# Performance work log

Measured on AMD Instinct MI355X. Metric: run time of the kernel, lower is better.

Reference implementation:

```python
import jax, jax.numpy as jnp
import numpy as np

ALPHA = 0.1  # config['alpha']


def setup_inputs() -> dict:
    key = jax.random.key(0)
    k1, k2, k3, k4, k5 = jax.random.split(key, 5)
    n_bs, bit, n_cls, class_bit, n_train = 128, 48, 100, 16, 10000
    u = jax.random.normal(k1, (n_bs, bit), dtype=jnp.float32)
    # multi-hot labels (float, as in torch: y.float())
    y = jax.random.bernoulli(k2, 0.1, (n_bs, n_cls)).astype(jnp.float32)
    ind = jnp.arange(n_bs, dtype=jnp.int64)  # distinct in-range row indices
    # buffers mid-training: U holds previous class-wise codes, Y previous labels
    U = jax.random.normal(k3, (n_train, n_cls, class_bit), dtype=jnp.float32) * 0.1
    Y = jax.random.bernoulli(k4, 0.1, (n_train, n_cls)).astype(jnp.float32)
    # xavier_uniform-like init for w_D [n_class, bit, class_bit]
    limit = np.sqrt(6.0 / (bit + class_bit)).astype(np.float32)
    w_D = jax.random.uniform(k5, (n_cls, bit, class_bit), dtype=jnp.float32,
                             minval=-limit, maxval=limit)
    return {"u": u, "y": y, "ind": ind, "U": U, "Y": Y, "w_D": w_D}


def reference(u, y, ind, U, Y, w_D):
    # update label buffer: self.Y[ind, :] = y
    Y = Y.at[ind].set(y)
    # u_ = matmul(u, w_D).permute(1,0,2): [n_bs, n_cls, class_bit]
    u_ = jnp.einsum('bk,ckd->bcd', u, w_D)
    # update code buffer with detached u_ (torch: self.U[ind] = u_.data)
    U = U.at[ind].set(jax.lax.stop_gradient(u_))
    # pairwise similarity s: [n_bs, n_train, n_cls]
    s = y[:, None, :] * Y[None, :, :]
    # inner_product: sum over class_bit -> [n_bs, n_train, n_cls]
    ip = jnp.einsum('tcd,bcd->btc', U, u_)
    # stable log(1 + exp(ip)) - s*ip, exactly as the torch expression
    likelihood = (jnp.log1p(jnp.exp(-jnp.abs(ip))) + jnp.maximum(ip, 0.0)
                  - s * ip).mean()
    quantization = ALPHA * jnp.mean((u_ - jnp.sign(u_)) ** 2)
    return likelihood + quantization
```

## Files before the change

kernel.cpp:

```cpp
#include <hip/hip_runtime.h>
#include <math.h>

#define CB 16
#define ALPHA 0.1f
#define LOG2E 1.4426950408889634f
#define LN2F  0.6931471805599453f
#define MAXW 8
#define N_BS 128
#define BIT  48

typedef __bf16 bf16x8 __attribute__((ext_vector_type(8)));
typedef float  f32x16 __attribute__((ext_vector_type(16)));

__device__ __forceinline__ unsigned int f2bf(float x) {
    unsigned int v = __float_as_uint(x);
    return (v + 0x7FFFu + ((v >> 16) & 1u)) >> 16;
}

__global__ __launch_bounds__(256, 4) void loss_fused(
        const float* __restrict__ u, const float* __restrict__ y,
        const float* __restrict__ w_D,
        const float* __restrict__ U, const float* __restrict__ Yb,
        const int* __restrict__ ind,
        float* __restrict__ partials, float* __restrict__ quant_partials,
        int n_cls, int n_train, int ntile, int GY) {
    __shared__ unsigned int ubf32[4 * N_BS * 9];
    __shared__ int pflag[MAXW * 32];

    const int tid  = threadIdx.x;
    const int lane = tid & 63;
    const int wid  = tid >> 6;
    const int bx   = blockIdx.x;
    const int by   = blockIdx.y;
    const int c    = bx * 4 + wid;
    const int r    = lane & 31;
    const int h    = lane >> 5;
    const int nw   = (ntile - by + GY - 1) / GY;

    pflag[tid] = -1;
    __syncthreads();
    if (tid < N_BS) {
        int t = ind[tid];
        for (int w = 0; w < nw; ++w) {
            unsigned rl = (unsigned)(t - (by + w * GY) * 32);
            if (rl < 32u) pflag[w * 32 + rl] = tid;
        }
    }

    float acc0[8] = {0,0,0,0,0,0,0,0};
    float acc1[8] = {0,0,0,0,0,0,0,0};
    float acc2[8] = {0,0,0,0,0,0,0,0};
    float acc3[8] = {0,0,0,0,0,0,0,0};
    {
        const float* __restrict__ wdc = w_D + (size_t)c * BIT * CB + h * 8;
        const float* __restrict__ ub0p = u + (size_t)(0 * 32 + r) * BIT;
        const float* __restrict__ ub1p = u + (size_t)(1 * 32 + r) * BIT;
        const float* __restrict__ ub2p = u + (size_t)(2 * 32 + r) * BIT;
        const float* __restrict__ ub3p = u + (size_t)(3 * 32 + r) * BIT;
        for (int k4 = 0; k4 < BIT / 4; ++k4) {
            float4 ub0 = *(const float4*)(ub0p + k4 * 4);
            float4 ub1 = *(const float4*)(ub1p + k4 * 4);
            float4 ub2 = *(const float4*)(ub2p + k4 * 4);
            float4 ub3 = *(const float4*)(ub3p + k4 * 4);
            #pragma unroll
            for (int kk = 0; kk < 4; ++kk) {
                const float* wrow = wdc + (k4 * 4 + kk) * CB;
                float4 wa = *(const float4*)(wrow);
                float4 wb = *(const float4*)(wrow + 4);
                float w8[8];
                w8[0]=wa.x; w8[1]=wa.y; w8[2]=wa.z; w8[3]=wa.w;
                w8[4]=wb.x; w8[5]=wb.y; w8[6]=wb.z; w8[7]=wb.w;
                float s0 = (&ub0.x)[kk], s1 = (&ub1.x)[kk];
                float s2 = (&ub2.x)[kk], s3 = (&ub3.x)[kk];
                #pragma unroll
                for (int j = 0; j < 8; ++j) {
                    acc0[j] = fmaf(s0, w8[j], acc0[j]);
                    acc1[j] = fmaf(s1, w8[j], acc1[j]);
                    acc2[j] = fmaf(s2, w8[j], acc2[j]);
                    acc3[j] = fmaf(s3, w8[j], acc3[j]);
                }
            }
        }
    }

    if (by == 0) {
        float q = 0.f;
        #pragma unroll
        for (int j = 0; j < 8; ++j) {
            float v, sgn, d;
            v = acc0[j]; sgn = (v>0.f)?1.f:((v<0.f)?-1.f:0.f); d = v-sgn; q = fmaf(d,d,q);
            v = acc1[j]; sgn = (v>0.f)?1.f:((v<0.f)?-1.f:0.f); d = v-sgn; q = fmaf(d,d,q);
            v = acc2[j]; sgn = (v>0.f)?1.f:((v<0.f)?-1.f:0.f); d = v-sgn; q = fmaf(d,d,q);
            v = acc3[j]; sgn = (v>0.f)?1.f:((v<0.f)?-1.f:0.f); d = v-sgn; q = fmaf(d,d,q);
        }
        #pragma unroll
        for (int off = 32; off > 0; off >>= 1) q += __shfl_down(q, off, 64);
        if (lane == 0) quant_partials[bx * 4 + wid] = q;
    }

    float ypc0 = y[(size_t)(0 * 32 + r) * n_cls + c];
    float ypc1 = y[(size_t)(1 * 32 + r) * n_cls + c];
    float ypc2 = y[(size_t)(2 * 32 + r) * n_cls + c];
    float ypc3 = y[(size_t)(3 * 32 + r) * n_cls + c];
    float vv[8], ww[8];
    #pragma unroll
    for (int j = 0; j < 8; ++j) {
        ww[j] = acc0[j] + acc1[j] + acc2[j] + acc3[j];
        vv[j] = ypc0*acc0[j] + ypc1*acc1[j] + ypc2*acc2[j] + ypc3*acc3[j];
    }
    #pragma unroll
    for (int m = 1; m < 32; m <<= 1) {
        #pragma unroll
        for (int j = 0; j < 8; ++j) {
            vv[j] += __shfl_xor(vv[j], m, 64);
            ww[j] += __shfl_xor(ww[j], m, 64);
        }
    }

    {
        unsigned int* d0 = &ubf32[(wid * N_BS + 0 * 32 + r) * 9 + h * 4];
        unsigned int* d1 = &ubf32[(wid * N_BS + 1 * 32 + r) * 9 + h * 4];
        unsigned int* d2 = &ubf32[(wid * N_BS + 2 * 32 + r) * 9 + h * 4];
        unsigned int* d3 = &ubf32[(wid * N_BS + 3 * 32 + r) * 9 + h * 4];
        #pragma unroll
        for (int j2 = 0; j2 < 4; ++j2) {
            d0[j2] = f2bf(acc0[2*j2]) | (f2bf(acc0[2*j2+1]) << 16);
            d1[j2] = f2bf(acc1[2*j2]) | (f2bf(acc1[2*j2+1]) << 16);
            d2[j2] = f2bf(acc2[2*j2]) | (f2bf(acc2[2*j2+1]) << 16);
            d3[j2] = f2bf(acc3[2*j2]) | (f2bf(acc3[2*j2+1]) << 16);
        }
    }

    bf16x8 B0, B1, B2, B3;
    #pragma unroll
    for (int j = 0; j < 8; ++j) {
        B0[j] = (__bf16)(acc0[j] * LOG2E);
        B1[j] = (__bf16)(acc1[j] * LOG2E);
        B2[j] = (__bf16)(acc2[j] * LOG2E);
        B3[j] = (__bf16)(acc3[j] * LOG2E);
    }

    __syncthreads();

    float acc = 0.f;
    f32x16 zc = {};
    #pragma unroll 1
    for (int w = 0; w < nw; ++w) {
        const int t0  = (by + w * GY) * 32;
        const int row = t0 + r;
        const int rc  = (row < n_train) ? row : (n_train - 1);
        const float* __restrict__ ar = U + ((size_t)rc * n_cls + c) * CB + h * 8;
        float4 a0 = *(const float4*)(ar);
        float4 a1 = *(const float4*)(ar + 4);
        float Yv = Yb[(size_t)rc * n_cls + c];

        const int pf = pflag[w * 32 + r];
        if (pf >= 0) {
            const unsigned int* src = &ubf32[(wid * N_BS + pf) * 9 + h * 4];
            unsigned int w0 = src[0], w1 = src[1], w2 = src[2], w3 = src[3];
            a0.x = __uint_as_float(w0 << 16);
            a0.y = __uint_as_float(w0 & 0xFFFF0000u);
            a0.z = __uint_as_float(w1 << 16);
            a0.w = __uint_as_float(w1 & 0xFFFF0000u);
            a1.x = __uint_as_float(w2 << 16);
            a1.y = __uint_as_float(w2 & 0xFFFF0000u);
            a1.z = __uint_as_float(w3 << 16);
            a1.w = __uint_as_float(w3 & 0xFFFF0000u);
            Yv = y[(size_t)pf * n_cls + c];
        }
        if (row >= n_train) {
            a0 = make_float4(0.f, 0.f, 0.f, 0.f); a1 = a0; Yv = 0.f;
        }

        float sv = a0.x*vv[0] + a0.y*vv[1] + a0.z*vv[2] + a0.w*vv[3]
                 + a1.x*vv[4] + a1.y*vv[5] + a1.z*vv[6] + a1.w*vv[7];
        float sw = a0.x*ww[0] + a0.y*ww[1] + a0.z*ww[2] + a0.w*ww[3]
                 + a1.x*ww[4] + a1.y*ww[5] + a1.z*ww[6] + a1.w*ww[7];

        bf16x8 A;
        A[0] = (__bf16)a0.x; A[1] = (__bf16)a0.y;
        A[2] = (__bf16)a0.z; A[3] = (__bf16)a0.w;
        A[4] = (__bf16)a1.x; A[5] = (__bf16)a1.y;
        A[6] = (__bf16)a1.z; A[7] = (__bf16)a1.w;

        float accA = 0.f;
        float pp   = 1.f;
        #pragma unroll
        for (int bt = 0; bt < 4; ++bt) {
            bf16x8 Bf = (bt == 0) ? B0 : (bt == 1) ? B1 : (bt == 2) ? B2 : B3;
            f32x16 D = __builtin_amdgcn_mfma_f32_32x32x16_bf16(A, Bf, zc,
                                                               0, 0, 0);
            float a[16];
            #pragma unroll
            for (int j = 0; j < 16; ++j) {
                float ipa = fabsf(D[j]);
                a[j] = 1.0f + __builtin_amdgcn_exp2f(-ipa);
                accA += ipa;
            }
            #pragma unroll
            for (int s = 1; s < 16; s <<= 1)
                #pragma unroll
                for (int j = 0; j < 16; j += 2 * s) a[j] *= a[j + s];
            pp *= a[0];
        }
        float accL = __builtin_amdgcn_logf(pp);
        acc += LN2F * accL + (0.5f * LN2F) * accA + 0.5f * sw - Yv * sv;
    }

    #pragma unroll
    for (int off = 32; off > 0; off >>= 1)
        acc += __shfl_down(acc, off, 64);
    if (lane == 0) {
        int bid = by * gridDim.x + bx;
        partials[bid * 4 + wid] = acc;
    }
}

__global__ __launch_bounds__(256) void finalize_kernel(
        const float* __restrict__ partials, int nblk,
        const float* __restrict__ quant_partials, int n_quant,
        float* __restrict__ out, double pad_corr,
        double like_scale, double quant_scale) {
    double s = 0.0, q = 0.0;
    for (int i = threadIdx.x; i < nblk; i += 256) s += (double)partials[i];
    for (int i = threadIdx.x; i < n_quant; i += 256) q += (double)quant_partials[i];
    #pragma unroll
    for (int off = 32; off > 0; off >>= 1) {
        s += __shfl_down(s, off, 64);
        q += __shfl_down(q, off, 64);
    }
    __shared__ double dred[4][2];
    int lane = threadIdx.x & 63, wid = threadIdx.x >> 6;
    if (lane == 0) { dred[wid][0] = s; dred[wid][1] = q; }
    __syncthreads();
    if (threadIdx.x == 0) {
        double S = dred[0][0] + dred[1][0] + dred[2][0] + dred[3][0];
        double Q = dred[0][1] + dred[1][1] + dred[2][1] + dred[3][1];
        out[0] = (float)((S - pad_corr) * like_scale + Q * quant_scale);
    }
}

extern "C" void kernel_launch(void* const* d_in, const int* in_sizes, int n_in,
                              void* d_out, int out_size, void* d_ws, size_t ws_size,
                              hipStream_t stream) {
    const float* u   = (const float*)d_in[0];
    const float* y   = (const float*)d_in[1];
    const int*   ind = (const int*)d_in[2];
    const float* U   = (const float*)d_in[3];
    const float* Yb  = (const float*)d_in[4];
    const float* w_D = (const float*)d_in[5];

    const int n_bs    = in_sizes[2];
    const int n_cls   = in_sizes[1] / n_bs;
    const int n_train = in_sizes[4] / n_cls;

    const int totalU = n_bs * n_cls * CB;
    const int ntile  = (n_train + 31) / 32;
    const int GY     = (ntile + MAXW - 1) / MAXW;
    const int gx     = (n_cls + 3) / 4;
    const int nblk   = GY * gx;
    const int npart  = nblk * 4;
    const int nquant = gx * 4;

    char* ws = (char*)d_ws;
    size_t off = 0;
    float* partials = (float*)(ws + off);        off += (size_t)npart * 4;
    float* quant_partials = (float*)(ws + off);  off += (size_t)nquant * 4;

    loss_fused<<<dim3(gx, GY), 256, 0, stream>>>(
        u, y, w_D, U, Yb, ind, partials, quant_partials,
        n_cls, n_train, ntile, GY);

    const double ln2 = 0.6931471805599453;
    const double n_pad = (double)((long long)(ntile * 32 - n_train) *
                                  (long long)n_bs * (long long)n_cls);
    const double pad_corr    = ln2 * n_pad;
    const double like_scale  = 1.0 / ((double)n_bs * n_train * n_cls);
    const double quant_scale = (double)ALPHA / (double)totalU;

    finalize_kernel<<<1, 256, 0, stream>>>(partials, npart,
                                           quant_partials, nquant,
                                           (float*)d_out, pad_corr,
                                           like_scale, quant_scale);
}
```

Before: 58.49 us.

## Stage u and w_D as bf16 in LDS and use packed FMA for projection

The kernel now cooperatively loads u and the block's w_D slice into shared memory as packed bf16 before the projection, instead of having every wave read them from global memory as fp32. The projection uses two-wide packed float math, and the shared buffer is reused for the bf16 code stash behind an extra barrier. The product tree for the log term becomes a serial running product, and MAXW shrinks to 4. This cuts redundant global traffic and instruction count in the prologue, but rounding u and w_D to bf16 reduces the accuracy of u_, and the serial product adds a longer dependency chain.

```diff
diff --git a/kernel.cpp b/kernel.cpp
--- a/kernel.cpp
+++ b/kernel.cpp
@@ -5,16 +5,23 @@
 #define ALPHA 0.1f
 #define LOG2E 1.4426950408889634f
 #define LN2F  0.6931471805599453f
-#define MAXW 8
+#define MAXW 4
 #define N_BS 128
 #define BIT  48
 
 typedef __bf16 bf16x8 __attribute__((ext_vector_type(8)));
 typedef float  f32x16 __attribute__((ext_vector_type(16)));
+typedef float  f32x2  __attribute__((ext_vector_type(2)));
 
 __device__ __forceinline__ unsigned int f2bf(float x) {
     unsigned int v = __float_as_uint(x);
     return (v + 0x7FFFu + ((v >> 16) & 1u)) >> 16;
+}
+__device__ __forceinline__ f32x2 bfup2(unsigned int p) {
+    f32x2 r;
+    r.x = __uint_as_float(p << 16);
+    r.y = __uint_as_float(p & 0xFFFF0000u);
+    return r;
 }
 
 __global__ __launch_bounds__(256, 4) void loss_fused(
@@ -24,8 +31,11 @@
         const int* __restrict__ ind,
         float* __restrict__ partials, float* __restrict__ quant_partials,
         int n_cls, int n_train, int ntile, int GY) {
-    __shared__ unsigned int ubf32[4 * N_BS * 9];
+    __shared__ unsigned int smem[4736];
     __shared__ int pflag[MAXW * 32];
+    unsigned int* u_st  = smem;
+    unsigned int* wd_st = smem + 3200;
+    unsigned int* ubf32 = smem;
 
     const int tid  = threadIdx.x;
     const int lane = tid & 63;
@@ -37,8 +47,24 @@
     const int h    = lane >> 5;
     const int nw   = (ntile - by + GY - 1) / GY;
 
-    pflag[tid] = -1;
+    if (tid < MAXW * 32) pflag[tid] = -1;
+    #pragma unroll
+    for (int it = 0; it < 12; ++it) {
+        int f = it * 256 + tid;
+        int b = f / 24, k2 = f % 24;
+        float2 uv = *(const float2*)(u + (size_t)b * BIT + k2 * 2);
+        u_st[b * 25 + k2] = f2bf(uv.x) | (f2bf(uv.y) << 16);
+    }
+    #pragma unroll
+    for (int it = 0; it < 6; ++it) {
+        int f = it * 256 + tid;
+        int cc = f / 384, rest = f % 384;
+        float2 wv = *(const float2*)(w_D + (size_t)(bx * 4 + cc) * BIT * CB
+                                     + rest * 2);
+        wd_st[f] = f2bf(wv.x) | (f2bf(wv.y) << 16);
+    }
     __syncthreads();
+
     if (tid < N_BS) {
         int t = ind[tid];
         for (int w = 0; w < nw; ++w) {
@@ -47,38 +73,40 @@
         }
     }
 
-    float acc0[8] = {0,0,0,0,0,0,0,0};
-    float acc1[8] = {0,0,0,0,0,0,0,0};
-    float acc2[8] = {0,0,0,0,0,0,0,0};
-    float acc3[8] = {0,0,0,0,0,0,0,0};
+    f32x2 acc0[4] = {}; f32x2 acc1[4] = {};
+    f32x2 acc2[4] = {}; f32x2 acc3[4] = {};
     {
-        const float* __restrict__ wdc = w_D + (size_t)c * BIT * CB + h * 8;
-        const float* __restrict__ ub0p = u + (size_t)(0 * 32 + r) * BIT;
-        const float* __restrict__ ub1p = u + (size_t)(1 * 32 + r) * BIT;
-        const float* __restrict__ ub2p = u + (size_t)(2 * 32 + r) * BIT;
-        const float* __restrict__ ub3p = u + (size_t)(3 * 32 + r) * BIT;
-        for (int k4 = 0; k4 < BIT / 4; ++k4) {
-            float4 ub0 = *(const float4*)(ub0p + k4 * 4);
-            float4 ub1 = *(const float4*)(ub1p + k4 * 4);
-            float4 ub2 = *(const float4*)(ub2p + k4 * 4);
-            float4 ub3 = *(const float4*)(ub3p + k4 * 4);
+        const unsigned int* __restrict__ up0 = u_st + (0 * 32 + r) * 25;
+        const unsigned int* __restrict__ up1 = u_st + (1 * 32 + r) * 25;
+        const unsigned int* __restrict__ up2 = u_st + (2 * 32 + r) * 25;
+        const unsigned int* __restrict__ up3 = u_st + (3 * 32 + r) * 25;
+        const unsigned int* __restrict__ wdc = wd_st + wid * 384 + h * 4;
+        for (int k2 = 0; k2 < 24; ++k2) {
+            unsigned int p0 = up0[k2], p1 = up1[k2];
+            unsigned int p2 = up2[k2], p3 = up3[k2];
             #pragma unroll
-            for (int kk = 0; kk < 4; ++kk) {
-                const float* wrow = wdc + (k4 * 4 + kk) * CB;
-                float4 wa = *(const float4*)(wrow);
-                float4 wb = *(const float4*)(wrow + 4);
-                float w8[8];
-                w8[0]=wa.x; w8[1]=wa.y; w8[2]=wa.z; w8[3]=wa.w;
-                w8[4]=wb.x; w8[5]=wb.y; w8[6]=wb.z; w8[7]=wb.w;
-                float s0 = (&ub0.x)[kk], s1 = (&ub1.x)[kk];
-                float s2 = (&ub2.x)[kk], s3 = (&ub3.x)[kk];
-                #pragma unroll
-                for (int j = 0; j < 8; ++j) {
-                    acc0[j] = fmaf(s0, w8[j], acc0[j]);
-                    acc1[j] = fmaf(s1, w8[j], acc1[j]);
-                    acc2[j] = fmaf(s2, w8[j], acc2[j]);
-                    acc3[j] = fmaf(s3, w8[j], acc3[j]);
-                }
+            for (int kk = 0; kk < 2; ++kk) {
+                uint4 wq = *(const uint4*)(wdc + (2 * k2 + kk) * 8);
+                f32x2 w0 = bfup2(wq.x), w1 = bfup2(wq.y);
+                f32x2 w2 = bfup2(wq.z), w3 = bfup2(wq.w);
+                float s0f = kk ? __uint_as_float(p0 & 0xFFFF0000u)
+                               : __uint_as_float(p0 << 16);
+                float s1f = kk ? __uint_as_float(p1 & 0xFFFF0000u)
+                               : __uint_as_float(p1 << 16);
+                float s2f = kk ? __uint_as_float(p2 & 0xFFFF0000u)
+                               : __uint_as_float(p2 << 16);
+                float s3f = kk ? __uint_as_float(p3 & 0xFFFF0000u)
+                               : __uint_as_float(p3 << 16);
+                f32x2 s0 = {s0f, s0f}, s1 = {s1f, s1f};
+                f32x2 s2 = {s2f, s2f}, s3 = {s3f, s3f};
+                acc0[0] += s0 * w0; acc0[1] += s0 * w1;
+                acc0[2] += s0 * w2; acc0[3] += s0 * w3;
+                acc1[0] += s1 * w0; acc1[1] += s1 * w1;
+                acc1[2] += s1 * w2; acc1[3] += s1 * w3;
+                acc2[0] += s2 * w0; acc2[1] += s2 * w1;
+                acc2[2] += s2 * w2; acc2[3] += s2 * w3;
+                acc3[0] += s3 * w0; acc3[1] += s3 * w1;
+                acc3[2] += s3 * w2; acc3[3] += s3 * w3;
             }
         }
     }
@@ -86,12 +114,16 @@
     if (by == 0) {
         float q = 0.f;
         #pragma unroll
-        for (int j = 0; j < 8; ++j) {
-            float v, sgn, d;
-            v = acc0[j]; sgn = (v>0.f)?1.f:((v<0.f)?-1.f:0.f); d = v-sgn; q = fmaf(d,d,q);
-            v = acc1[j]; sgn = (v>0.f)?1.f:((v<0.f)?-1.f:0.f); d = v-sgn; q = fmaf(d,d,q);
-            v = acc2[j]; sgn = (v>0.f)?1.f:((v<0.f)?-1.f:0.f); d = v-sgn; q = fmaf(d,d,q);
-            v = acc3[j]; sgn = (v>0.f)?1.f:((v<0.f)?-1.f:0.f); d = v-sgn; q = fmaf(d,d,q);
+        for (int j2 = 0; j2 < 4; ++j2) {
+            float vb[8] = {acc0[j2].x, acc0[j2].y, acc1[j2].x, acc1[j2].y,
+                           acc2[j2].x, acc2[j2].y, acc3[j2].x, acc3[j2].y};
+            #pragma unroll
+            for (int i = 0; i < 8; ++i) {
+                float v = vb[i];
+                float sg = (v > 0.f) ? 1.f : ((v < 0.f) ? -1.f : 0.f);
+                float d = v - sg;
+                q = fmaf(d, d, q);
+            }
         }
         #pragma unroll
         for (int off = 32; off > 0; off >>= 1) q += __shfl_down(q, off, 64);
@@ -102,20 +134,45 @@
     float ypc1 = y[(size_t)(1 * 32 + r) * n_cls + c];
     float ypc2 = y[(size_t)(2 * 32 + r) * n_cls + c];
     float ypc3 = y[(size_t)(3 * 32 + r) * n_cls + c];
-    float vv[8], ww[8];
-    #pragma unroll
-    for (int j = 0; j < 8; ++j) {
-        ww[j] = acc0[j] + acc1[j] + acc2[j] + acc3[j];
-        vv[j] = ypc0*acc0[j] + ypc1*acc1[j] + ypc2*acc2[j] + ypc3*acc3[j];
+    f32x2 y0 = {ypc0, ypc0}, y1 = {ypc1, ypc1};
+    f32x2 y2 = {ypc2, ypc2}, y3 = {ypc3, ypc3};
+    f32x2 vv[4], ww[4];
+    #pragma unroll
+    for (int j2 = 0; j2 < 4; ++j2) {
+        ww[j2] = acc0[j2] + acc1[j2] + acc2[j2] + acc3[j2];
+        vv[j2] = y0 * acc0[j2] + y1 * acc1[j2] + y2 * acc2[j2] + y3 * acc3[j2];
     }
     #pragma unroll
     for (int m = 1; m < 32; m <<= 1) {
         #pragma unroll
-        for (int j = 0; j < 8; ++j) {
-            vv[j] += __shfl_xor(vv[j], m, 64);
-            ww[j] += __shfl_xor(ww[j], m, 64);
-        }
-    }
+        for (int j2 = 0; j2 < 4; ++j2) {
+            vv[j2].x += __shfl_xor(vv[j2].x, m, 64);
+            vv[j2].y += __shfl_xor(vv[j2].y, m, 64);
+            ww[j2].x += __shfl_xor(ww[j2].x, m, 64);
+            ww[j2].y += __shfl_xor(ww[j2].y, m, 64);
+        }
+    }
+    float vvf[8], wwf[8];
+    #pragma unroll
+    for (int j2 = 0; j2 < 4; ++j2) {
+        vvf[2 * j2] = vv[j2].x; vvf[2 * j2 + 1] = vv[j2].y;
+        wwf[2 * j2] = ww[j2].x; wwf[2 * j2 + 1] = ww[j2].y;
+    }
+
+    bf16x8 B0, B1, B2, B3;
+    #pragma unroll
+    for (int j2 = 0; j2 < 4; ++j2) {
+        B0[2 * j2] = (__bf16)(acc0[j2].x * LOG2E);
+        B0[2 * j2 + 1] = (__bf16)(acc0[j2].y * LOG2E);
+        B1[2 * j2] = (__bf16)(acc1[j2].x * LOG2E);
+        B1[2 * j2 + 1] = (__bf16)(acc1[j2].y * LOG2E);
+        B2[2 * j2] = (__bf16)(acc2[j2].x * LOG2E);
+        B2[2 * j2 + 1] = (__bf16)(acc2[j2].y * LOG2E);
+        B3[2 * j2] = (__bf16)(acc3[j2].x * LOG2E);
+        B3[2 * j2 + 1] = (__bf16)(acc3[j2].y * LOG2E);
+    }
+
+    __syncthreads();
 
     {
         unsigned int* d0 = &ubf32[(wid * N_BS + 0 * 32 + r) * 9 + h * 4];
@@ -124,22 +181,12 @@
         unsigned int* d3 = &ubf32[(wid * N_BS + 3 * 32 + r) * 9 + h * 4];
         #pragma unroll
         for (int j2 = 0; j2 < 4; ++j2) {
-            d0[j2] = f2bf(acc0[2*j2]) | (f2bf(acc0[2*j2+1]) << 16);
-            d1[j2] = f2bf(acc1[2*j2]) | (f2bf(acc1[2*j2+1]) << 16);
-            d2[j2] = f2bf(acc2[2*j2]) | (f2bf(acc2[2*j2+1]) << 16);
-            d3[j2] = f2bf(acc3[2*j2]) | (f2bf(acc3[2*j2+1]) << 16);
-        }
-    }
-
-    bf16x8 B0, B1, B2, B3;
-    #pragma unroll
-    for (int j = 0; j < 8; ++j) {
-        B0[j] = (__bf16)(acc0[j] * LOG2E);
-        B1[j] = (__bf16)(acc1[j] * LOG2E);
-        B2[j] = (__bf16)(acc2[j] * LOG2E);
-        B3[j] = (__bf16)(acc3[j] * LOG2E);
-    }
-
+            d0[j2] = f2bf(acc0[j2].x) | (f2bf(acc0[j2].y) << 16);
+            d1[j2] = f2bf(acc1[j2].x) | (f2bf(acc1[j2].y) << 16);
+            d2[j2] = f2bf(acc2[j2].x) | (f2bf(acc2[j2].y) << 16);
+            d3[j2] = f2bf(acc3[j2].x) | (f2bf(acc3[j2].y) << 16);
+        }
+    }
     __syncthreads();
 
     float acc = 0.f;
@@ -172,10 +219,10 @@
             a0 = make_float4(0.f, 0.f, 0.f, 0.f); a1 = a0; Yv = 0.f;
         }
 
-        float sv = a0.x*vv[0] + a0.y*vv[1] + a0.z*vv[2] + a0.w*vv[3]
-                 + a1.x*vv[4] + a1.y*vv[5] + a1.z*vv[6] + a1.w*vv[7];
-        float sw = a0.x*ww[0] + a0.y*ww[1] + a0.z*ww[2] + a0.w*ww[3]
-                 + a1.x*ww[4] + a1.y*ww[5] + a1.z*ww[6] + a1.w*ww[7];
+        float sv = a0.x*vvf[0] + a0.y*vvf[1] + a0.z*vvf[2] + a0.w*vvf[3]
+                 + a1.x*vvf[4] + a1.y*vvf[5] + a1.z*vvf[6] + a1.w*vvf[7];
+        float sw = a0.x*wwf[0] + a0.y*wwf[1] + a0.z*wwf[2] + a0.w*wwf[3]
+                 + a1.x*wwf[4] + a1.y*wwf[5] + a1.z*wwf[6] + a1.w*wwf[7];
 
         bf16x8 A;
         A[0] = (__bf16)a0.x; A[1] = (__bf16)a0.y;
@@ -190,18 +237,12 @@
             bf16x8 Bf = (bt == 0) ? B0 : (bt == 1) ? B1 : (bt == 2) ? B2 : B3;
             f32x16 D = __builtin_amdgcn_mfma_f32_32x32x16_bf16(A, Bf, zc,
                                                                0, 0, 0);
-            float a[16];
             #pragma unroll
             for (int j = 0; j < 16; ++j) {
                 float ipa = fabsf(D[j]);
-                a[j] = 1.0f + __builtin_amdgcn_exp2f(-ipa);
                 accA += ipa;
+                pp *= (1.0f + __builtin_amdgcn_exp2f(-ipa));
             }
-            #pragma unroll
-            for (int s = 1; s < 16; s <<= 1)
-                #pragma unroll
-                for (int j = 0; j < 16; j += 2 * s) a[j] *= a[j + s];
-            pp *= a[0];
         }
         float accL = __builtin_amdgcn_logf(pp);
         acc += LN2F * accL + (0.5f * LN2F) * accA + 0.5f * sw - Yv * sv;
```

New measurement: 67.51 us. 1.15x slower.

## Compute u·w_D projection with MFMA via LDS-staged bf16 weights

Applied to the files above, without the earlier changes.

Replaces the scalar FMA projection of u by w_D with bf16 MFMA instructions, staging a transposed bf16 copy of each block's w_D slice in shared memory. The per-class code slice is written to LDS from the MFMA output, and the y-weighted and plain column sums are recomputed from LDS. The LOG2E scale moves from the B operand onto the A operand, and MAXW is reduced so the pflag loop is fully unrolled. The aim is to cut the per-block prologue cost of the FP32 projection, at the price of extra LDS traffic, a wasted half of the MFMA N dimension, and bf16 rounding of u and w_D.

```diff
diff --git a/kernel.cpp b/kernel.cpp
--- a/kernel.cpp
+++ b/kernel.cpp
@@ -5,7 +5,7 @@
 #define ALPHA 0.1f
 #define LOG2E 1.4426950408889634f
 #define LN2F  0.6931471805599453f
-#define MAXW 8
+#define MAXW 4
 #define N_BS 128
 #define BIT  48
 
@@ -24,7 +24,8 @@
         const int* __restrict__ ind,
         float* __restrict__ partials, float* __restrict__ quant_partials,
         int n_cls, int n_train, int ntile, int GY) {
-    __shared__ unsigned int ubf32[4 * N_BS * 9];
+    __shared__ unsigned int slice[4 * N_BS * 9];
+    __shared__ unsigned int wdt[4 * 16 * 25];
     __shared__ int pflag[MAXW * 32];
 
     const int tid  = threadIdx.x;
@@ -37,113 +38,112 @@
     const int h    = lane >> 5;
     const int nw   = (ntile - by + GY - 1) / GY;
 
-    pflag[tid] = -1;
+    if (tid < MAXW * 32) pflag[tid] = -1;
+    unsigned short* wdt16w = (unsigned short*)wdt;
+    #pragma unroll
+    for (int it = 0; it < 12; ++it) {
+        int f = it * 256 + tid;
+        int cc = f / 768, rem = f % 768;
+        int k = rem >> 4, d = rem & 15;
+        float wv = w_D[(size_t)(bx * 4 + cc) * 768 + rem];
+        wdt16w[(cc * 16 + d) * 50 + k] = (unsigned short)f2bf(wv);
+    }
     __syncthreads();
+
     if (tid < N_BS) {
         int t = ind[tid];
-        for (int w = 0; w < nw; ++w) {
+        #pragma unroll
+        for (int w = 0; w < MAXW; ++w) {
             unsigned rl = (unsigned)(t - (by + w * GY) * 32);
             if (rl < 32u) pflag[w * 32 + rl] = tid;
         }
     }
 
-    float acc0[8] = {0,0,0,0,0,0,0,0};
-    float acc1[8] = {0,0,0,0,0,0,0,0};
-    float acc2[8] = {0,0,0,0,0,0,0,0};
-    float acc3[8] = {0,0,0,0,0,0,0,0};
+    unsigned short* sl16 = (unsigned short*)slice;
+    const int dcol = lane & 31;
+    float qacc = 0.f;
+    f32x16 zc = {};
+    #pragma unroll 1
+    for (int bt = 0; bt < 4; ++bt) {
+        const int b0 = bt * 32 + r;
+        f32x16 D = zc;
+        #pragma unroll
+        for (int kt = 0; kt < 3; ++kt) {
+            const float* __restrict__ up = u + (size_t)b0 * BIT + kt * 16 + h * 8;
+            float4 ua = *(const float4*)(up);
+            float4 ub = *(const float4*)(up + 4);
+            bf16x8 Af;
+            Af[0] = (__bf16)ua.x; Af[1] = (__bf16)ua.y;
+            Af[2] = (__bf16)ua.z; Af[3] = (__bf16)ua.w;
+            Af[4] = (__bf16)ub.x; Af[5] = (__bf16)ub.y;
+            Af[6] = (__bf16)ub.z; Af[7] = (__bf16)ub.w;
+            union { unsigned int u32[4]; bf16x8 v; } B;
+            B.u32[0] = 0; B.u32[1] = 0; B.u32[2] = 0; B.u32[3] = 0;
+            if (r < 16) {
+                const unsigned int* src = &wdt[(wid * 16 + r) * 25 + kt * 8 + h * 4];
+                B.u32[0] = src[0]; B.u32[1] = src[1];
+                B.u32[2] = src[2]; B.u32[3] = src[3];
+            }
+            D = __builtin_amdgcn_mfma_f32_32x32x16_bf16(Af, B.v, D, 0, 0, 0);
+        }
+        if (by == 0) {
+            #pragma unroll
+            for (int i = 0; i < 16; ++i) {
+                float v = D[i];
+                float sg = (v > 0.f) ? 1.f : ((v < 0.f) ? -1.f : 0.f);
+                float dd = v - sg;
+                qacc = fmaf(dd, dd, qacc);
+            }
+        }
+        if (dcol < 16) {
+            #pragma unroll
+            for (int i = 0; i < 16; ++i) {
+                int row = (i & 3) + 8 * (i >> 2) + 4 * h;
+                sl16[(wid * N_BS + bt * 32 + row) * 18 + dcol] =
+                    (unsigned short)f2bf(D[i]);
+            }
+        }
+    }
+    if (by == 0) {
+        #pragma unroll
+        for (int off = 32; off > 0; off >>= 1) qacc += __shfl_down(qacc, off, 64);
+        if (lane == 0) quant_partials[bx * 4 + wid] = qacc;
+    }
+
+    float vvf[8], wwf[8];
     {
-        const float* __restrict__ wdc = w_D + (size_t)c * BIT * CB + h * 8;
-        const float* __restrict__ ub0p = u + (size_t)(0 * 32 + r) * BIT;
-        const float* __restrict__ ub1p = u + (size_t)(1 * 32 + r) * BIT;
-        const float* __restrict__ ub2p = u + (size_t)(2 * 32 + r) * BIT;
-        const float* __restrict__ ub3p = u + (size_t)(3 * 32 + r) * BIT;
-        for (int k4 = 0; k4 < BIT / 4; ++k4) {
-            float4 ub0 = *(const float4*)(ub0p + k4 * 4);
-            float4 ub1 = *(const float4*)(ub1p + k4 * 4);
-            float4 ub2 = *(const float4*)(ub2p + k4 * 4);
-            float4 ub3 = *(const float4*)(ub3p + k4 * 4);
-            #pragma unroll
-            for (int kk = 0; kk < 4; ++kk) {
-                const float* wrow = wdc + (k4 * 4 + kk) * CB;
-                float4 wa = *(const float4*)(wrow);
-                float4 wb = *(const float4*)(wrow + 4);
-                float w8[8];
-                w8[0]=wa.x; w8[1]=wa.y; w8[2]=wa.z; w8[3]=wa.w;
-                w8[4]=wb.x; w8[5]=wb.y; w8[6]=wb.z; w8[7]=wb.w;
-                float s0 = (&ub0.x)[kk], s1 = (&ub1.x)[kk];
-                float s2 = (&ub2.x)[kk], s3 = (&ub3.x)[kk];
-                #pragma unroll
-                for (int j = 0; j < 8; ++j) {
-                    acc0[j] = fmaf(s0, w8[j], acc0[j]);
-                    acc1[j] = fmaf(s1, w8[j], acc1[j]);
-                    acc2[j] = fmaf(s2, w8[j], acc2[j]);
-                    acc3[j] = fmaf(s3, w8[j], acc3[j]);
-                }
-            }
-        }
-    }
-
-    if (by == 0) {
-        float q = 0.f;
+        const int dd = lane & 15, g = lane >> 4;
+        float vv = 0.f, ww = 0.f;
+        #pragma unroll 4
+        for (int bb = 0; bb < 32; ++bb) {
+            int b = g * 32 + bb;
+            float uv = __uint_as_float(
+                ((unsigned int)sl16[(wid * N_BS + b) * 18 + dd]) << 16);
+            ww += uv;
+            vv = fmaf(y[(size_t)b * n_cls + c], uv, vv);
+        }
+        vv += __shfl_xor(vv, 16, 64); vv += __shfl_xor(vv, 32, 64);
+        ww += __shfl_xor(ww, 16, 64); ww += __shfl_xor(ww, 32, 64);
         #pragma unroll
         for (int j = 0; j < 8; ++j) {
-            float v, sgn, d;
-            v = acc0[j]; sgn = (v>0.f)?1.f:((v<0.f)?-1.f:0.f); d = v-sgn; q = fmaf(d,d,q);
-            v = acc1[j]; sgn = (v>0.f)?1.f:((v<0.f)?-1.f:0.f); d = v-sgn; q = fmaf(d,d,q);
-            v = acc2[j]; sgn = (v>0.f)?1.f:((v<0.f)?-1.f:0.f); d = v-sgn; q = fmaf(d,d,q);
-            v = acc3[j]; sgn = (v>0.f)?1.f:((v<0.f)?-1.f:0.f); d = v-sgn; q = fmaf(d,d,q);
-        }
-        #pragma unroll
-        for (int off = 32; off > 0; off >>= 1) q += __shfl_down(q, off, 64);
-        if (lane == 0) quant_partials[bx * 4 + wid] = q;
-    }
-
-    float ypc0 = y[(size_t)(0 * 32 + r) * n_cls + c];
-    float ypc1 = y[(size_t)(1 * 32 + r) * n_cls + c];
-    float ypc2 = y[(size_t)(2 * 32 + r) * n_cls + c];
-    float ypc3 = y[(size_t)(3 * 32 + r) * n_cls + c];
-    float vv[8], ww[8];
-    #pragma unroll
-    for (int j = 0; j < 8; ++j) {
-        ww[j] = acc0[j] + acc1[j] + acc2[j] + acc3[j];
-        vv[j] = ypc0*acc0[j] + ypc1*acc1[j] + ypc2*acc2[j] + ypc3*acc3[j];
-    }
-    #pragma unroll
-    for (int m = 1; m < 32; m <<= 1) {
-        #pragma unroll
-        for (int j = 0; j < 8; ++j) {
-            vv[j] += __shfl_xor(vv[j], m, 64);
-            ww[j] += __shfl_xor(ww[j], m, 64);
-        }
-    }
-
-    {
-        unsigned int* d0 = &ubf32[(wid * N_BS + 0 * 32 + r) * 9 + h * 4];
-        unsigned int* d1 = &ubf32[(wid * N_BS + 1 * 32 + r) * 9 + h * 4];
-        unsigned int* d2 = &ubf32[(wid * N_BS + 2 * 32 + r) * 9 + h * 4];
-        unsigned int* d3 = &ubf32[(wid * N_BS + 3 * 32 + r) * 9 + h * 4];
-        #pragma unroll
-        for (int j2 = 0; j2 < 4; ++j2) {
-            d0[j2] = f2bf(acc0[2*j2]) | (f2bf(acc0[2*j2+1]) << 16);
-            d1[j2] = f2bf(acc1[2*j2]) | (f2bf(acc1[2*j2+1]) << 16);
-            d2[j2] = f2bf(acc2[2*j2]) | (f2bf(acc2[2*j2+1]) << 16);
-            d3[j2] = f2bf(acc3[2*j2]) | (f2bf(acc3[2*j2+1]) << 16);
-        }
-    }
-
-    bf16x8 B0, B1, B2, B3;
-    #pragma unroll
-    for (int j = 0; j < 8; ++j) {
-        B0[j] = (__bf16)(acc0[j] * LOG2E);
-        B1[j] = (__bf16)(acc1[j] * LOG2E);
-        B2[j] = (__bf16)(acc2[j] * LOG2E);
-        B3[j] = (__bf16)(acc3[j] * LOG2E);
+            vvf[j] = __shfl(vv, h * 8 + j, 64);
+            wwf[j] = __shfl(ww, h * 8 + j, 64);
+        }
+    }
+
+    bf16x8 BF[4];
+    #pragma unroll
+    for (int bt = 0; bt < 4; ++bt) {
+        const unsigned int* src = &slice[(wid * N_BS + bt * 32 + r) * 9 + h * 4];
+        union { unsigned int u32[4]; bf16x8 v; } B;
+        B.u32[0] = src[0]; B.u32[1] = src[1];
+        B.u32[2] = src[2]; B.u32[3] = src[3];
+        BF[bt] = B.v;
     }
 
     __syncthreads();
 
     float acc = 0.f;
-    f32x16 zc = {};
     #pragma unroll 1
     for (int w = 0; w < nw; ++w) {
         const int t0  = (by + w * GY) * 32;
@@ -156,7 +156,7 @@
 
         const int pf = pflag[w * 32 + r];
         if (pf >= 0) {
-            const unsigned int* src = &ubf32[(wid * N_BS + pf) * 9 + h * 4];
+            const unsigned int* src = &slice[(wid * N_BS + pf) * 9 + h * 4];
             unsigned int w0 = src[0], w1 = src[1], w2 = src[2], w3 = src[3];
             a0.x = __uint_as_float(w0 << 16);
             a0.y = __uint_as_float(w0 & 0xFFFF0000u);
@@ -172,36 +172,36 @@
             a0 = make_float4(0.f, 0.f, 0.f, 0.f); a1 = a0; Yv = 0.f;
         }
 
-        float sv = a0.x*vv[0] + a0.y*vv[1] + a0.z*vv[2] + a0.w*vv[3]
-                 + a1.x*vv[4] + a1.y*vv[5] + a1.z*vv[6] + a1.w*vv[7];
-        float sw = a0.x*ww[0] + a0.y*ww[1] + a0.z*ww[2] + a0.w*ww[3]
-                 + a1.x*ww[4] + a1.y*ww[5] + a1.z*ww[6] + a1.w*ww[7];
+        float sv = a0.x*vvf[0] + a0.y*vvf[1] + a0.z*vvf[2] + a0.w*vvf[3]
+                 + a1.x*vvf[4] + a1.y*vvf[5] + a1.z*vvf[6] + a1.w*vvf[7];
+        float sw = a0.x*wwf[0] + a0.y*wwf[1] + a0.z*wwf[2] + a0.w*wwf[3]
+                 + a1.x*wwf[4] + a1.y*wwf[5] + a1.z*wwf[6] + a1.w*wwf[7];
 
         bf16x8 A;
-        A[0] = (__bf16)a0.x; A[1] = (__bf16)a0.y;
-        A[2] = (__bf16)a0.z; A[3] = (__bf16)a0.w;
-        A[4] = (__bf16)a1.x; A[5] = (__bf16)a1.y;
-        A[6] = (__bf16)a1.z; A[7] = (__bf16)a1.w;
+        A[0] = (__bf16)(a0.x * LOG2E); A[1] = (__bf16)(a0.y * LOG2E);
+        A[2] = (__bf16)(a0.z * LOG2E); A[3] = (__bf16)(a0.w * LOG2E);
+        A[4] = (__bf16)(a1.x * LOG2E); A[5] = (__bf16)(a1.y * LOG2E);
+        A[6] = (__bf16)(a1.z * LOG2E); A[7] = (__bf16)(a1.w * LOG2E);
 
         float accA = 0.f;
         float pp   = 1.f;
         #pragma unroll
         for (int bt = 0; bt < 4; ++bt) {
-            bf16x8 Bf = (bt == 0) ? B0 : (bt == 1) ? B1 : (bt == 2) ? B2 : B3;
-            f32x16 D = __builtin_amdgcn_mfma_f32_32x32x16_bf16(A, Bf, zc,
+            f32x16 D = __builtin_amdgcn_mfma_f32_32x32x16_bf16(A, BF[bt], zc,
                                                                0, 0, 0);
-            float a[16];
             #pragma unroll
-            for (int j = 0; j < 16; ++j) {
-                float ipa = fabsf(D[j]);
-                a[j] = 1.0f + __builtin_amdgcn_exp2f(-ipa);
-                accA += ipa;
-            }
-            #pragma unroll
-            for (int s = 1; s < 16; s <<= 1)
+            for (int half = 0; half < 2; ++half) {
+                float a[8];
                 #pragma unroll
-                for (int j = 0; j < 16; j += 2 * s) a[j] *= a[j + s];
-            pp *= a[0];
+                for (int j = 0; j < 8; ++j) {
+                    float ipa = fabsf(D[half * 8 + j]);
+                    a[j] = 1.0f + __builtin_amdgcn_exp2f(-ipa);
+                    accA += ipa;
+                }
+                a[0] *= a[1]; a[2] *= a[3]; a[4] *= a[5]; a[6] *= a[7];
+                a[0] *= a[2]; a[4] *= a[6];
+                pp *= a[0] * a[4];
+            }
         }
         float accL = __builtin_amdgcn_logf(pp);
         acc += LN2F * accL + (0.5f * LN2F) * accA + 0.5f * sw - Yv * sv;
```

Measured after the change: 53.24 us. 1.1x faster.
